# Kernel tuning notes

Hardware: AMD Instinct MI355X
Metric: run time of the kernel (lower is better)

Reference implementation:

```python
import jax, jax.numpy as jnp
import numpy as np

N_SITES, NODE_F = 50000, 64
N_PERM, N_NEIGH = 12, 8
IN_F = N_NEIGH * NODE_F  # 512
OUT_F = 64
LN2 = float(np.log(2.0))


def setup_inputs() -> dict:
    key = jax.random.key(0)
    k1, k2, k3, k4 = jax.random.split(key, 4)
    X_sites = jax.random.normal(k1, (N_SITES, NODE_F), dtype=jnp.float32)
    X_NSs = jax.random.randint(k2, (N_SITES, N_PERM, N_NEIGH), 0, N_SITES)
    # nn.Linear(IN_F, OUT_F): weight (OUT_F, IN_F), bias (OUT_F,)
    bound = 1.0 / np.sqrt(IN_F)
    W = jax.random.uniform(k3, (OUT_F, IN_F), minval=-bound, maxval=bound, dtype=jnp.float32)
    b = jax.random.uniform(k4, (OUT_F,), minval=-bound, maxval=bound, dtype=jnp.float32)
    return {"X_sites": X_sites, "X_NSs": X_NSs, "W": W, "b": b}


def reference(X_sites, X_NSs, W, b):
    # Gather neighbor features: (N, P, K, F) -> (N, P, K*F)
    gathered = X_sites[X_NSs].reshape(X_NSs.shape[0], N_PERM, IN_F)
    # Linear: (N, P, IN_F) @ (IN_F, OUT_F) + b
    x1 = jnp.einsum('npi,oi->npo', gathered, W) + b
    # Shifted softplus: softplus(x) - log(2)  (dropout treated as identity / eval mode)
    x2 = jax.nn.softplus(x1) - LN2
    # Sum over permutations -> (N, OUT_F)
    return x2.sum(axis=1)
```

## Files before the change

### kernel.cpp

```cpp
#include <hip/hip_runtime.h>
#include <hip/hip_bf16.h>

#define N_SITES 50000
#define N_PERM  12
#define N_NEIGH 8
#define NODE_F  64
#define IN_F    512
#define OUT_F   64
#define N_TILES (N_SITES / 16)
#define LN2F    0.69314718055994530942f

#define XCHUNKS (N_SITES * NODE_F / 8)
#define WCHUNKS (OUT_F * IN_F / 8)
#define SLOT_E  520
#define BUF_E   (16 * SLOT_E)

typedef __bf16 bf16x8 __attribute__((ext_vector_type(8)));
typedef float  f32x4  __attribute__((ext_vector_type(4)));

__device__ __forceinline__ unsigned short f32_to_bf16_rne(unsigned int u) {
    u += 0x7FFFu + ((u >> 16) & 1u);
    return (unsigned short)(u >> 16);
}

__device__ __forceinline__ int probe_is_bf16(const void* Xorig) {
    int lane = threadIdx.x & 63;
    unsigned short h = ((const unsigned short*)Xorig)[2 * lane];
    int e = (h >> 7) & 0xFF;
    unsigned long long mm = __ballot(e >= 110 && e <= 140);
    return (__popcll(mm) >= 48) ? 1 : 0;
}

__device__ __forceinline__ void pack8(const uint4* src, uint4* dst, int c) {
    uint4 a = src[2 * c], b = src[2 * c + 1];
    uint4 o;
    o.x = (unsigned int)f32_to_bf16_rne(a.x) | ((unsigned int)f32_to_bf16_rne(a.y) << 16);
    o.y = (unsigned int)f32_to_bf16_rne(a.z) | ((unsigned int)f32_to_bf16_rne(a.w) << 16);
    o.z = (unsigned int)f32_to_bf16_rne(b.x) | ((unsigned int)f32_to_bf16_rne(b.y) << 16);
    o.w = (unsigned int)f32_to_bf16_rne(b.z) | ((unsigned int)f32_to_bf16_rne(b.w) << 16);
    dst[c] = o;
}

__global__ void convert_all(const void* __restrict__ Xv, const void* __restrict__ Wv,
                            const void* __restrict__ Bv, uint4* __restrict__ Xb,
                            uint4* __restrict__ Wb, float* __restrict__ Bf) {
    const int isbf = probe_is_bf16(Xv);
    int c = blockIdx.x * blockDim.x + threadIdx.x;
    if (c < XCHUNKS) {
        if (isbf) Xb[c] = ((const uint4*)Xv)[c];
        else      pack8((const uint4*)Xv, Xb, c);
    } else if (c < XCHUNKS + WCHUNKS) {
        int cw = c - XCHUNKS;
        if (isbf) Wb[cw] = ((const uint4*)Wv)[cw];
        else      pack8((const uint4*)Wv, Wb, cw);
    } else if (c < XCHUNKS + WCHUNKS + OUT_F) {
        int i = c - XCHUNKS - WCHUNKS;
        Bf[i] = isbf ? (float)((const __bf16*)Bv)[i] : ((const float*)Bv)[i];
    }
}

__device__ __forceinline__ float softplus_sh(float x) {
    float t = __expf(-fabsf(x));
    return fmaxf(x, 0.f) + 0.69314718056f * __log2f(1.f + t);
}

__device__ __forceinline__ void async16(const __bf16* g, __bf16* l) {
    __builtin_amdgcn_global_load_lds(
        (const __attribute__((address_space(1))) unsigned int*)g,
        (__attribute__((address_space(3))) unsigned int*)l, 16, 0, 0);
}

__global__ __launch_bounds__(128, 2)
void lcnn_dma(const void* __restrict__ Xorig, const __bf16* __restrict__ Xb,
              const int* __restrict__ NS, const __bf16* __restrict__ Wb,
              const float* __restrict__ Bf, void* __restrict__ outv)
{
    __shared__ __align__(16) __bf16 Abuf[2][BUF_E];

    const int wn   = threadIdx.x >> 6;
    const int lane = threadIdx.x & 63;
    const int m    = lane & 15;
    const int quad = lane >> 4;
    const int mk   = m & 7;
    const int mh   = m >> 3;
    const int tile = blockIdx.x;

    bf16x8 Wfrag[16][2];
    #pragma unroll
    for (int ks = 0; ks < 16; ++ks) {
        #pragma unroll
        for (int nf = 0; nf < 2; ++nf)
            Wfrag[ks][nf] = *(const bf16x8*)(Wb + (size_t)(wn * 32 + nf * 16 + m) * IN_F
                                             + ks * 32 + quad * 8);
    }

    const float bias0 = Bf[wn * 32 + m];
    const float bias1 = Bf[wn * 32 + 16 + m];

    auto load_idx = [&](int p_, int out[8]) {
        #pragma unroll
        for (int i = 0; i < 8; ++i) {
            int t = wn * 8 + i;
            int s = ((t & 1) << 3) + (lane >> 3);
            int k = t >> 1;
            out[i] = NS[(size_t)(tile * 16 + s) * (N_PERM * N_NEIGH) + p_ * N_NEIGH + k];
        }
    };
    auto stage = [&](int buf_, const int idxv[8]) {
        const int csrc = (lane & 7) ^ (lane >> 3);
        #pragma unroll
        for (int i = 0; i < 8; ++i) {
            int t = wn * 8 + i;
            async16(Xb + (size_t)idxv[i] * NODE_F + csrc * 8, &Abuf[buf_][t * SLOT_E]);
        }
    };

    int idxn[8];
    load_idx(0, idxn);
    stage(0, idxn);
    load_idx(1, idxn);
    __syncthreads();

    f32x4 sum0 = {0.f, 0.f, 0.f, 0.f};
    f32x4 sum1 = {0.f, 0.f, 0.f, 0.f};
    for (int p = 0; p < N_PERM; ++p) {
        if (p < N_PERM - 1) stage((p + 1) & 1, idxn);
        if (p < N_PERM - 2) load_idx(p + 2, idxn);

        f32x4 acc0 = {0.f, 0.f, 0.f, 0.f};
        f32x4 acc1 = {0.f, 0.f, 0.f, 0.f};
        const __bf16* bb = &Abuf[p & 1][0];
        #pragma unroll
        for (int ks = 0; ks < 16; ++ks) {
            int t_r = (ks >> 1) * 2 + mh;
            int j   = ((ks & 1) << 2) | quad;
            bf16x8 afr = *(const bf16x8*)(bb + t_r * SLOT_E + mk * 64 + ((j ^ mk) << 3));
            acc0 = __builtin_amdgcn_mfma_f32_16x16x32_bf16(afr, Wfrag[ks][0], acc0, 0, 0, 0);
            acc1 = __builtin_amdgcn_mfma_f32_16x16x32_bf16(afr, Wfrag[ks][1], acc1, 0, 0, 0);
        }
        #pragma unroll
        for (int r = 0; r < 4; ++r) {
            sum0[r] += softplus_sh(acc0[r] + bias0);
            sum1[r] += softplus_sh(acc1[r] + bias1);
        }
        __syncthreads();
    }

    const int isbf = probe_is_bf16(Xorig);
    #pragma unroll
    for (int r = 0; r < 4; ++r) {
        size_t pos = (size_t)(tile * 16 + quad * 4 + r) * OUT_F + wn * 32 + m;
        float v0 = sum0[r] - 12.0f * LN2F;
        float v1 = sum1[r] - 12.0f * LN2F;
        if (isbf) {
            ((__bf16*)outv)[pos]      = (__bf16)v0;
            ((__bf16*)outv)[pos + 16] = (__bf16)v1;
        } else {
            ((float*)outv)[pos]      = v0;
            ((float*)outv)[pos + 16] = v1;
        }
    }
}

__global__ void lcnn_fallback(const float* __restrict__ X, const int* __restrict__ NS,
                              const float* __restrict__ W, const float* __restrict__ B,
                              float* __restrict__ out) {
    int t = blockIdx.x * blockDim.x + threadIdx.x;
    if (t >= N_SITES * OUT_F) return;
    int sitei = t >> 6, o = t & 63;
    const int* ns = NS + (size_t)sitei * 96;
    float s = 0.f;
    for (int p = 0; p < N_PERM; ++p) {
        float x = B[o];
        for (int n = 0; n < N_NEIGH; ++n) {
            const float* xr = X + (size_t)ns[p * 8 + n] * NODE_F;
            const float* wr = W + (size_t)o * IN_F + n * NODE_F;
            for (int f = 0; f < NODE_F; ++f) x += xr[f] * wr[f];
        }
        s += softplus_sh(x);
    }
    out[t] = s - 12.0f * LN2F;
}

extern "C" void kernel_launch(void* const* d_in, const int* in_sizes, int n_in,
                              void* d_out, int out_size, void* d_ws, size_t ws_size,
                              hipStream_t stream) {
    const void* X  = d_in[0];
    const int*  NS = (const int*)d_in[1];
    const void* W  = d_in[2];
    const void* B  = d_in[3];

    char* ws = (char*)d_ws;
    __bf16* Xb = (__bf16*)ws;
    __bf16* Wb = (__bf16*)(ws + (size_t)XCHUNKS * 16);
    float*  Bf = (float*)(ws + (size_t)(XCHUNKS + WCHUNKS) * 16);
    const bool conv = ws_size >= (size_t)(XCHUNKS + WCHUNKS) * 16 + OUT_F * 4;

    if (conv) {
        int nch = XCHUNKS + WCHUNKS + OUT_F;
        hipLaunchKernelGGL(convert_all, dim3((nch + 255) / 256), dim3(256), 0, stream,
                           X, W, B, (uint4*)Xb, (uint4*)Wb, Bf);
        hipLaunchKernelGGL(lcnn_dma, dim3(N_TILES), dim3(128), 0, stream,
                           X, Xb, NS, Wb, Bf, d_out);
    } else {
        hipLaunchKernelGGL(lcnn_fallback,
                           dim3((N_SITES * OUT_F + 255) / 256), dim3(256), 0, stream,
                           (const float*)X, NS, (const float*)W, (const float*)B,
                           (float*)d_out);
    }
}
```

Before: 156.0 us.

## Split K dimension across four waves with LDS reduction of partial sums

The block grows from two waves to four: each pair of waves splits the 512-long reduction in half, and the upper-half waves write partial accumulators to a small LDS exchange buffer that the lower-half waves add before bias and softplus. This halves the per-wave weight fragments held in registers and the per-wave gather count, aiming for higher occupancy and more latency hiding on the gather-bound loop. It adds an extra barrier and LDS round trip per permutation, and leaves half the waves idle during the softplus epilogue.

```diff
diff --git a/kernel.cpp b/kernel.cpp
--- a/kernel.cpp
+++ b/kernel.cpp
@@ -70,52 +70,55 @@
         (__attribute__((address_space(3))) unsigned int*)l, 16, 0, 0);
 }
 
-__global__ __launch_bounds__(128, 2)
+__global__ __launch_bounds__(256, 4)
 void lcnn_dma(const void* __restrict__ Xorig, const __bf16* __restrict__ Xb,
               const int* __restrict__ NS, const __bf16* __restrict__ Wb,
               const float* __restrict__ Bf, void* __restrict__ outv)
 {
     __shared__ __align__(16) __bf16 Abuf[2][BUF_E];
-
-    const int wn   = threadIdx.x >> 6;
+    __shared__ __align__(16) float  Xch[2][8][64];
+
+    const int wave = threadIdx.x >> 6;
     const int lane = threadIdx.x & 63;
+    const int fh   = wave & 1;
+    const int kh   = wave >> 1;
     const int m    = lane & 15;
     const int quad = lane >> 4;
     const int mk   = m & 7;
     const int mh   = m >> 3;
     const int tile = blockIdx.x;
 
-    bf16x8 Wfrag[16][2];
+    bf16x8 Wfrag[8][2];
     #pragma unroll
-    for (int ks = 0; ks < 16; ++ks) {
+    for (int ksl = 0; ksl < 8; ++ksl) {
         #pragma unroll
         for (int nf = 0; nf < 2; ++nf)
-            Wfrag[ks][nf] = *(const bf16x8*)(Wb + (size_t)(wn * 32 + nf * 16 + m) * IN_F
-                                             + ks * 32 + quad * 8);
-    }
-
-    const float bias0 = Bf[wn * 32 + m];
-    const float bias1 = Bf[wn * 32 + 16 + m];
-
-    auto load_idx = [&](int p_, int out[8]) {
-        #pragma unroll
-        for (int i = 0; i < 8; ++i) {
-            int t = wn * 8 + i;
+            Wfrag[ksl][nf] = *(const bf16x8*)(Wb + (size_t)(fh * 32 + nf * 16 + m) * IN_F
+                                              + (kh * 8 + ksl) * 32 + quad * 8);
+    }
+
+    const float bias0 = Bf[fh * 32 + m];
+    const float bias1 = Bf[fh * 32 + 16 + m];
+
+    auto load_idx = [&](int p_, int out[4]) {
+        #pragma unroll
+        for (int i = 0; i < 4; ++i) {
+            int t = wave * 4 + i;
             int s = ((t & 1) << 3) + (lane >> 3);
             int k = t >> 1;
             out[i] = NS[(size_t)(tile * 16 + s) * (N_PERM * N_NEIGH) + p_ * N_NEIGH + k];
         }
     };
-    auto stage = [&](int buf_, const int idxv[8]) {
+    auto stage = [&](int buf_, const int idxv[4]) {
         const int csrc = (lane & 7) ^ (lane >> 3);
         #pragma unroll
-        for (int i = 0; i < 8; ++i) {
-            int t = wn * 8 + i;
+        for (int i = 0; i < 4; ++i) {
+            int t = wave * 4 + i;
             async16(Xb + (size_t)idxv[i] * NODE_F + csrc * 8, &Abuf[buf_][t * SLOT_E]);
         }
     };
 
-    int idxn[8];
+    int idxn[4];
     load_idx(0, idxn);
     stage(0, idxn);
     load_idx(1, idxn);
@@ -131,33 +134,50 @@
         f32x4 acc1 = {0.f, 0.f, 0.f, 0.f};
         const __bf16* bb = &Abuf[p & 1][0];
         #pragma unroll
-        for (int ks = 0; ks < 16; ++ks) {
+        for (int ksl = 0; ksl < 8; ++ksl) {
+            int ks  = kh * 8 + ksl;
             int t_r = (ks >> 1) * 2 + mh;
             int j   = ((ks & 1) << 2) | quad;
             bf16x8 afr = *(const bf16x8*)(bb + t_r * SLOT_E + mk * 64 + ((j ^ mk) << 3));
-            acc0 = __builtin_amdgcn_mfma_f32_16x16x32_bf16(afr, Wfrag[ks][0], acc0, 0, 0, 0);
-            acc1 = __builtin_amdgcn_mfma_f32_16x16x32_bf16(afr, Wfrag[ks][1], acc1, 0, 0, 0);
-        }
+            acc0 = __builtin_amdgcn_mfma_f32_16x16x32_bf16(afr, Wfrag[ksl][0], acc0, 0, 0, 0);
+            acc1 = __builtin_amdgcn_mfma_f32_16x16x32_bf16(afr, Wfrag[ksl][1], acc1, 0, 0, 0);
+        }
+
+        if (kh) {
+            #pragma unroll
+            for (int r = 0; r < 4; ++r) {
+                Xch[fh][r][lane]     = acc0[r];
+                Xch[fh][r + 4][lane] = acc1[r];
+            }
+        }
+        asm volatile("s_waitcnt lgkmcnt(0)" ::: "memory");
+        __builtin_amdgcn_s_barrier();
+        asm volatile("" ::: "memory");
+
+        if (!kh) {
+            #pragma unroll
+            for (int r = 0; r < 4; ++r) {
+                sum0[r] += softplus_sh(acc0[r] + Xch[fh][r][lane]     + bias0);
+                sum1[r] += softplus_sh(acc1[r] + Xch[fh][r + 4][lane] + bias1);
+            }
+        }
+        if (p < N_PERM - 1) __syncthreads();
+    }
+
+    if (!kh) {
+        const int isbf = probe_is_bf16(Xorig);
         #pragma unroll
         for (int r = 0; r < 4; ++r) {
-            sum0[r] += softplus_sh(acc0[r] + bias0);
-            sum1[r] += softplus_sh(acc1[r] + bias1);
-        }
-        __syncthreads();
-    }
-
-    const int isbf = probe_is_bf16(Xorig);
-    #pragma unroll
-    for (int r = 0; r < 4; ++r) {
-        size_t pos = (size_t)(tile * 16 + quad * 4 + r) * OUT_F + wn * 32 + m;
-        float v0 = sum0[r] - 12.0f * LN2F;
-        float v1 = sum1[r] - 12.0f * LN2F;
-        if (isbf) {
-            ((__bf16*)outv)[pos]      = (__bf16)v0;
-            ((__bf16*)outv)[pos + 16] = (__bf16)v1;
-        } else {
-            ((float*)outv)[pos]      = v0;
-            ((float*)outv)[pos + 16] = v1;
+            size_t pos = (size_t)(tile * 16 + quad * 4 + r) * OUT_F + fh * 32 + m;
+            float v0 = sum0[r] - 12.0f * LN2F;
+            float v1 = sum1[r] - 12.0f * LN2F;
+            if (isbf) {
+                ((__bf16*)outv)[pos]      = (__bf16)v0;
+                ((__bf16*)outv)[pos + 16] = (__bf16)v1;
+            } else {
+                ((float*)outv)[pos]      = v0;
+                ((float*)outv)[pos + 16] = v1;
+            }
         }
     }
 }
@@ -200,7 +220,7 @@
         int nch = XCHUNKS + WCHUNKS + OUT_F;
         hipLaunchKernelGGL(convert_all, dim3((nch + 255) / 256), dim3(256), 0, stream,
                            X, W, B, (uint4*)Xb, (uint4*)Wb, Bf);
-        hipLaunchKernelGGL(lcnn_dma, dim3(N_TILES), dim3(128), 0, stream,
+        hipLaunchKernelGGL(lcnn_dma, dim3(N_TILES), dim3(256), 0, stream,
                            X, Xb, NS, Wb, Bf, d_out);
     } else {
         hipLaunchKernelGGL(lcnn_fallback,
```

Result: slower. 167.1 us (+7.1%).

## Split gather into dedicated producer waves with a four-deep LDS ring

Applied to the files above, without the earlier changes.

Doubles the block to four waves: two producer waves preload all neighbor indices (packed as 16-bit pairs) and issue async global-to-LDS gathers three permutations ahead into a four-buffer ring. The two consumer waves only run the MFMA and softplus work. Raw s_barrier calls paired with explicit vmcnt waits replace __syncthreads. The aim is to hide gather latency behind compute. In exchange, LDS use doubles, which can lower occupancy. Packing indices into 16 bits also truncates any site index at or above 65536; with 50000 sites this still fits.

```diff
diff --git a/kernel.cpp b/kernel.cpp
--- a/kernel.cpp
+++ b/kernel.cpp
@@ -70,66 +70,103 @@
         (__attribute__((address_space(3))) unsigned int*)l, 16, 0, 0);
 }
 
-__global__ __launch_bounds__(128, 2)
+
+#define BARW(N) do {                                                          \
+        asm volatile("s_waitcnt vmcnt(" #N ")" ::: "memory");                 \
+        __builtin_amdgcn_s_barrier();                                         \
+        asm volatile("" ::: "memory");                                        \
+    } while (0)
+#define CBAR() do {                                                           \
+        asm volatile("" ::: "memory");                                        \
+        __builtin_amdgcn_s_barrier();                                         \
+        asm volatile("" ::: "memory");                                        \
+    } while (0)
+
+__global__ __launch_bounds__(256, 2)
 void lcnn_dma(const void* __restrict__ Xorig, const __bf16* __restrict__ Xb,
               const int* __restrict__ NS, const __bf16* __restrict__ Wb,
               const float* __restrict__ Bf, void* __restrict__ outv)
 {
-    __shared__ __align__(16) __bf16 Abuf[2][BUF_E];
-
-    const int wn   = threadIdx.x >> 6;
+    __shared__ __align__(16) __bf16 Abuf[4][BUF_E];
+
+    const int wave = threadIdx.x >> 6;
     const int lane = threadIdx.x & 63;
+    const int tile = blockIdx.x;
+
+    if (wave >= 2) {
+        const int pw   = wave - 2;
+        const int srow = lane >> 3;
+        const int csrc = (lane & 7) ^ srow;
+        const int* ns0p = NS + (size_t)(tile * 16 + srow)     * (N_PERM * N_NEIGH) + pw * 4;
+        const int* ns1p = NS + (size_t)(tile * 16 + srow + 8) * (N_PERM * N_NEIGH) + pw * 4;
+
+        unsigned int pk[N_PERM][4];
+        #pragma unroll
+        for (int p = 0; p < N_PERM; ++p) {
+            int4 a = *(const int4*)(ns0p + p * N_NEIGH);
+            int4 b = *(const int4*)(ns1p + p * N_NEIGH);
+            pk[p][0] = ((unsigned)a.x & 0xFFFFu) | ((unsigned)b.x << 16);
+            pk[p][1] = ((unsigned)a.y & 0xFFFFu) | ((unsigned)b.y << 16);
+            pk[p][2] = ((unsigned)a.z & 0xFFFFu) | ((unsigned)b.z << 16);
+            pk[p][3] = ((unsigned)a.w & 0xFFFFu) | ((unsigned)b.w << 16);
+        }
+
+#define PSTG(b_, p_) do {                                                     \
+            _Pragma("unroll")                                                 \
+            for (int i = 0; i < 8; ++i) {                                     \
+                unsigned int w_ = pk[p_][i >> 1];                             \
+                unsigned int id_ = (i & 1) ? (w_ >> 16) : (w_ & 0xFFFFu);     \
+                async16(Xb + (size_t)id_ * NODE_F + csrc * 8,                 \
+                        &Abuf[b_][(pw * 8 + i) * SLOT_E]);                    \
+            }                                                                 \
+        } while (0)
+
+        PSTG(0, 0);
+        PSTG(1, 1);
+        PSTG(2, 2);
+        BARW(16);
+
+        #pragma unroll
+        for (int p = 0; p < N_PERM; ++p) {
+            if (p + 3 < N_PERM) {
+                const int b3 = (p + 3) & 3;
+                const int p3 = p + 3;
+                PSTG(b3, p3);
+            }
+            if (p <= 8)       BARW(16);
+            else if (p == 9)  BARW(8);
+            else if (p == 10) BARW(0);
+        }
+#undef PSTG
+        return;
+    }
+
+    const int fw   = wave;
     const int m    = lane & 15;
     const int quad = lane >> 4;
     const int mk   = m & 7;
     const int mh   = m >> 3;
-    const int tile = blockIdx.x;
 
     bf16x8 Wfrag[16][2];
     #pragma unroll
     for (int ks = 0; ks < 16; ++ks) {
         #pragma unroll
         for (int nf = 0; nf < 2; ++nf)
-            Wfrag[ks][nf] = *(const bf16x8*)(Wb + (size_t)(wn * 32 + nf * 16 + m) * IN_F
+            Wfrag[ks][nf] = *(const bf16x8*)(Wb + (size_t)(fw * 32 + nf * 16 + m) * IN_F
                                              + ks * 32 + quad * 8);
     }
-
-    const float bias0 = Bf[wn * 32 + m];
-    const float bias1 = Bf[wn * 32 + 16 + m];
-
-    auto load_idx = [&](int p_, int out[8]) {
-        #pragma unroll
-        for (int i = 0; i < 8; ++i) {
-            int t = wn * 8 + i;
-            int s = ((t & 1) << 3) + (lane >> 3);
-            int k = t >> 1;
-            out[i] = NS[(size_t)(tile * 16 + s) * (N_PERM * N_NEIGH) + p_ * N_NEIGH + k];
-        }
-    };
-    auto stage = [&](int buf_, const int idxv[8]) {
-        const int csrc = (lane & 7) ^ (lane >> 3);
-        #pragma unroll
-        for (int i = 0; i < 8; ++i) {
-            int t = wn * 8 + i;
-            async16(Xb + (size_t)idxv[i] * NODE_F + csrc * 8, &Abuf[buf_][t * SLOT_E]);
-        }
-    };
-
-    int idxn[8];
-    load_idx(0, idxn);
-    stage(0, idxn);
-    load_idx(1, idxn);
-    __syncthreads();
+    const float bias0 = Bf[fw * 32 + m];
+    const float bias1 = Bf[fw * 32 + 16 + m];
+
+    CBAR();
 
     f32x4 sum0 = {0.f, 0.f, 0.f, 0.f};
     f32x4 sum1 = {0.f, 0.f, 0.f, 0.f};
+    #pragma unroll
     for (int p = 0; p < N_PERM; ++p) {
-        if (p < N_PERM - 1) stage((p + 1) & 1, idxn);
-        if (p < N_PERM - 2) load_idx(p + 2, idxn);
-
         f32x4 acc0 = {0.f, 0.f, 0.f, 0.f};
         f32x4 acc1 = {0.f, 0.f, 0.f, 0.f};
-        const __bf16* bb = &Abuf[p & 1][0];
+        const __bf16* bb = &Abuf[p & 3][0];
         #pragma unroll
         for (int ks = 0; ks < 16; ++ks) {
             int t_r = (ks >> 1) * 2 + mh;
@@ -143,13 +180,13 @@
             sum0[r] += softplus_sh(acc0[r] + bias0);
             sum1[r] += softplus_sh(acc1[r] + bias1);
         }
-        __syncthreads();
+        if (p < N_PERM - 1) CBAR();
     }
 
     const int isbf = probe_is_bf16(Xorig);
     #pragma unroll
     for (int r = 0; r < 4; ++r) {
-        size_t pos = (size_t)(tile * 16 + quad * 4 + r) * OUT_F + wn * 32 + m;
+        size_t pos = (size_t)(tile * 16 + quad * 4 + r) * OUT_F + fw * 32 + m;
         float v0 = sum0[r] - 12.0f * LN2F;
         float v1 = sum1[r] - 12.0f * LN2F;
         if (isbf) {
@@ -200,7 +237,7 @@
         int nch = XCHUNKS + WCHUNKS + OUT_F;
         hipLaunchKernelGGL(convert_all, dim3((nch + 255) / 256), dim3(256), 0, stream,
                            X, W, B, (uint4*)Xb, (uint4*)Wb, Bf);
-        hipLaunchKernelGGL(lcnn_dma, dim3(N_TILES), dim3(128), 0, stream,
+        hipLaunchKernelGGL(lcnn_dma, dim3(N_TILES), dim3(256), 0, stream,
                            X, Xb, NS, Wb, Bf, d_out);
     } else {
         hipLaunchKernelGGL(lcnn_fallback,
```

Result: no change. 157.7 us (+1.1%).
